# Optimization experiments

Measured on AMD Instinct MI355X. Metric: run time of the kernel, lower is better.

## Reference

```python
import jax, jax.numpy as jnp
import numpy as np

H, HK, D, WIN = 16, 4, 128, 1024  # n_head, n_kv_head, head_dim, left window


def rmsnorm(x):
    eps = jnp.asarray(jnp.finfo(x.dtype).eps, x.dtype)
    return x * jax.lax.rsqrt(jnp.mean(x * x, axis=-1, keepdims=True) + eps)


def rope(x, cos, sin):
    d = x.shape[-1] // 2
    x1, x2 = x[..., :d], x[..., d:]
    return jnp.concatenate([x1 * cos + x2 * sin, x1 * -sin + x2 * cos], axis=-1)


def setup_inputs() -> dict:
    key = jax.random.key(0)
    ks = jax.random.split(key, 12)
    B, T, C = 4, 2048, 2048
    t = jnp.arange(T, dtype=jnp.float32)[:, None]
    inv = 1.0 / (10000.0 ** (jnp.arange(D // 2, dtype=jnp.float32) / (D // 2)))
    ang = t * inv[None, :]  # [T, D/2]
    return {
        "x": jax.random.normal(ks[0], (B, T, C), jnp.float32),
        "x0": jax.random.normal(ks[1], (B, T, C), jnp.float32),
        "ve": jnp.zeros((B, T, C), jnp.float32),  # unused in add_init_qkv branch
        "cos": jnp.cos(ang)[None, :, None, :],  # [1,T,1,D/2]
        "sin": jnp.sin(ang)[None, :, None, :],
        "Wq": jax.random.normal(ks[2], (H * D, C), jnp.float32) * 0.02,
        "Wk": jax.random.normal(ks[3], (HK * D, C), jnp.float32) * 0.02,
        "Wv": jax.random.normal(ks[4], (HK * D, C), jnp.float32) * 0.02,
        "Wproj": jax.random.normal(ks[5], (C, H * D), jnp.float32) * 0.02,
        "alpha_q": jnp.ones((1,), jnp.float32),
        "beta_q": jax.random.uniform(ks[6], (1,), jnp.float32),
        "alpha_k": jnp.ones((1,), jnp.float32),
        "beta_k": jax.random.uniform(ks[7], (1,), jnp.float32),
        "alpha_v": jnp.ones((1,), jnp.float32),
        "beta_v": jax.random.uniform(ks[8], (1,), jnp.float32),
    }


def reference(x, x0, ve, cos, sin, Wq, Wk, Wv, Wproj,
              alpha_q, beta_q, alpha_k, beta_k, alpha_v, beta_v):
    B, T, C = x.shape
    g = H // HK  # GQA group size

    q = (x @ Wq.T).reshape(B, T, H, D)
    k = (x @ Wk.T).reshape(B, T, HK, D)
    v = (x @ Wv.T).reshape(B, T, HK, D)
    v_init = v

    # is_target + add_init_qkv + learn_init_coeffs: blend with projections of norm(x0)
    x0n = rmsnorm(x0)
    cqx = (x0n @ Wq.T).reshape(B, T, H, D)
    ckx = (x0n @ Wk.T).reshape(B, T, HK, D)
    cvx = (x0n @ Wv.T).reshape(B, T, HK, D)
    q = alpha_q * q + beta_q * cqx
    k = alpha_k * k + beta_k * ckx
    v = alpha_v * v + beta_v * cvx

    # rotary + qk-norm + 1.2 scale
    q = rmsnorm(rope(q, cos, sin)) * 1.2
    k = rmsnorm(rope(k, cos, sin)) * 1.2

    qg = q.reshape(B, T, HK, g, D)
    scale = 1.0 / np.sqrt(D)
    scores = jnp.einsum('bqhgd,bkhd->bhgqk', qg, k) * scale  # [B,HK,g,T,T]
    i = jnp.arange(T)[:, None]
    j = jnp.arange(T)[None, :]
    mask = (j <= i) & (i - j <= WIN)
    scores = jnp.where(mask, scores, -jnp.inf)
    p = jax.nn.softmax(scores, axis=-1)
    y = jnp.einsum('bhgqk,bkhd->bqhgd', p, v).reshape(B, T, H * D)

    y = y @ Wproj.T
    return (y, v_init)
```

## Files before the change

### kernel.cpp

```cpp
#include <hip/hip_runtime.h>
#include <hip/hip_bf16.h>
#include <math.h>


using bf16 = __hip_bfloat16;
typedef __attribute__((ext_vector_type(8))) short bf16x8;
typedef __attribute__((ext_vector_type(4))) short bf16x4;
typedef __attribute__((ext_vector_type(4))) float f32x4;

constexpr int Bb = 4, Ts = 2048, Cc = 2048, NH = 16, NKV = 4, Dh = 128, WIN = 1024;
constexpr float EPS = 1.1920929e-07f;

__device__ __forceinline__ void gld16(void* lds, const void* g) {
  __builtin_amdgcn_global_load_lds(
      (__attribute__((address_space(1))) unsigned int*)((void*)g),
      (__attribute__((address_space(3))) unsigned int*)lds, 16, 0, 0);
}

__device__ __forceinline__ unsigned short bfbits(float f) {
  bf16 h = __float2bfloat16(f);
  return __builtin_bit_cast(unsigned short, h);
}

__device__ __forceinline__ void store_out(float* p, float v) { *p = v; }
__device__ __forceinline__ void store_out(bf16* p, float v) { *p = __float2bfloat16(v); }

__device__ __forceinline__ f32x4 mfma16(bf16x4 a, bf16x4 b, f32x4 c) {
#if __has_builtin(__builtin_amdgcn_mfma_f32_16x16x16bf16_1k)
  return __builtin_amdgcn_mfma_f32_16x16x16bf16_1k(a, b, c, 0, 0, 0);
#else
  bf16x8 a8 = {a[0], a[1], a[2], a[3], 0, 0, 0, 0};
  bf16x8 b8 = {b[0], b[1], b[2], b[3], 0, 0, 0, 0};
  return __builtin_amdgcn_mfma_f32_16x16x32_bf16(a8, b8, c, 0, 0, 0);
#endif
}

__global__ __launch_bounds__(256) void convert_w(const float* __restrict__ src,
                                                 bf16* __restrict__ dst, int n4) {
  int i = blockIdx.x * 256 + threadIdx.x;
  if (i < n4) {
    float4 v = ((const float4*)src)[i];
    ushort4 u;
    u.x = bfbits(v.x); u.y = bfbits(v.y); u.z = bfbits(v.z); u.w = bfbits(v.w);
    ((ushort4*)dst)[i] = u;
  }
}

__global__ __launch_bounds__(256) void prep(
    const float* __restrict__ x, const float* __restrict__ x0,
    const float* aq_p, const float* bq_p, const float* ak_p, const float* bk_p,
    bf16* __restrict__ xq, bf16* __restrict__ xk,
    bf16* __restrict__ xb, bf16* __restrict__ x0n) {
  const int row = blockIdx.x, tid = threadIdx.x;
  const float4* xr = (const float4*)(x + (size_t)row * Cc);
  const float4* nr = (const float4*)(x0 + (size_t)row * Cc);
  float4 xa[2], na[2];
  float ss = 0.f;
#pragma unroll
  for (int j = 0; j < 2; ++j) {
    xa[j] = xr[tid + j * 256];
    na[j] = nr[tid + j * 256];
    ss += na[j].x * na[j].x + na[j].y * na[j].y + na[j].z * na[j].z + na[j].w * na[j].w;
  }
#pragma unroll
  for (int o = 32; o; o >>= 1) ss += __shfl_xor(ss, o);
  __shared__ float red[4];
  if ((tid & 63) == 0) red[tid >> 6] = ss;
  __syncthreads();
  const float rms = rsqrtf((red[0] + red[1] + red[2] + red[3]) * (1.f / Cc) + EPS);
  const float aq = *aq_p, bq = *bq_p, ak = *ak_p, bk = *bk_p;
#pragma unroll
  for (int j = 0; j < 2; ++j) {
    const size_t base = (size_t)row * Cc + (size_t)(tid + j * 256) * 4;
    float nx[4] = {na[j].x * rms, na[j].y * rms, na[j].z * rms, na[j].w * rms};
    float xv[4] = {xa[j].x, xa[j].y, xa[j].z, xa[j].w};
    ushort4 uq, uk, ub, un;
    uq.x = bfbits(aq * xv[0] + bq * nx[0]); uq.y = bfbits(aq * xv[1] + bq * nx[1]);
    uq.z = bfbits(aq * xv[2] + bq * nx[2]); uq.w = bfbits(aq * xv[3] + bq * nx[3]);
    uk.x = bfbits(ak * xv[0] + bk * nx[0]); uk.y = bfbits(ak * xv[1] + bk * nx[1]);
    uk.z = bfbits(ak * xv[2] + bk * nx[2]); uk.w = bfbits(ak * xv[3] + bk * nx[3]);
    ub.x = bfbits(xv[0]); ub.y = bfbits(xv[1]); ub.z = bfbits(xv[2]); ub.w = bfbits(xv[3]);
    un.x = bfbits(nx[0]); un.y = bfbits(nx[1]); un.z = bfbits(nx[2]); un.w = bfbits(nx[3]);
    *(ushort4*)(xq + base) = uq;
    *(ushort4*)(xk + base) = uk;
    *(ushort4*)(xb + base) = ub;
    *(ushort4*)(x0n + base) = un;
  }
}

template <typename OutT>
__device__ __forceinline__ void gemm_body(
    const bf16* __restrict__ A, const bf16* __restrict__ W,
    OutT* __restrict__ C, int N, int K) {
  __shared__ unsigned short sA[128 * 64];
  __shared__ unsigned short sB[128 * 64];
  const int tid = threadIdx.x, wave = tid >> 6, lane = tid & 63;
  const int quad = lane >> 4, l15 = lane & 15;
  const int bm = blockIdx.x * 128, bn = blockIdx.y * 128;
  const int wm = (wave >> 1) * 64, wn = (wave & 1) * 64;
  const int srow = wave * 32 + (lane >> 3);
  const int scol = (lane & 7) * 8;

  f32x4 acc[4][4] = {};

  for (int k0 = 0; k0 < K; k0 += 64) {
#pragma unroll
    for (int i = 0; i < 4; ++i) {
      gld16(&sA[(wave * 32 + i * 8) * 64], &A[(size_t)(bm + srow + i * 8) * K + k0 + scol]);
      gld16(&sB[(wave * 32 + i * 8) * 64], &W[(size_t)(bn + srow + i * 8) * K + k0 + scol]);
    }
    __syncthreads();
#pragma unroll
    for (int kk = 0; kk < 2; ++kk) {
      bf16x8 af[4], bfr[4];
#pragma unroll
      for (int t = 0; t < 4; ++t)
        af[t] = *(const bf16x8*)&sA[(wm + t * 16 + l15) * 64 + kk * 32 + quad * 8];
#pragma unroll
      for (int t = 0; t < 4; ++t)
        bfr[t] = *(const bf16x8*)&sB[(wn + t * 16 + l15) * 64 + kk * 32 + quad * 8];
#pragma unroll
      for (int tm = 0; tm < 4; ++tm)
#pragma unroll
        for (int tn = 0; tn < 4; ++tn)
          acc[tm][tn] = __builtin_amdgcn_mfma_f32_16x16x32_bf16(af[tm], bfr[tn], acc[tm][tn], 0, 0, 0);
    }
    __syncthreads();
  }
#pragma unroll
  for (int tm = 0; tm < 4; ++tm)
#pragma unroll
    for (int tn = 0; tn < 4; ++tn)
#pragma unroll
      for (int r = 0; r < 4; ++r) {
        const int row = bm + wm + tm * 16 + quad * 4 + r;
        const int col = bn + wn + tn * 16 + l15;
        store_out(&C[(size_t)row * N + col], acc[tm][tn][r]);
      }
}

template <typename OutT>
__global__ __launch_bounds__(256) void gemm_bt(
    const bf16* __restrict__ A, const bf16* __restrict__ W,
    OutT* __restrict__ C, int N, int K) {
  gemm_body<OutT>(A, W, C, N, K);
}

struct GemmTriple { const bf16* A; const bf16* W; bf16* C; };
struct GemmTriple3 { GemmTriple t[3]; };

__global__ __launch_bounds__(256) void gemm_bt3(GemmTriple3 g, int N, int K) {
  const GemmTriple tr = g.t[blockIdx.z];
  gemm_body<bf16>(tr.A, tr.W, tr.C, N, K);
}

__global__ __launch_bounds__(256) void post_qk(
    const bf16* __restrict__ pre, const float* __restrict__ cosp,
    const float* __restrict__ sinp, bf16* __restrict__ outh, int nh, float mult) {
  const int wid = blockIdx.x * 4 + (threadIdx.x >> 6);
  const int lane = threadIdx.x & 63;
  const int h = wid % nh;
  const int bt = wid / nh;
  const int t = bt & (Ts - 1);
  const int b = bt >> 11;
  const size_t src = (size_t)bt * (size_t)(nh * Dh) + (size_t)h * Dh;
  float x1 = __bfloat162float(pre[src + lane]);
  float x2 = __bfloat162float(pre[src + 64 + lane]);
  float c = cosp[t * 64 + lane], s = sinp[t * 64 + lane];
  float o1 = x1 * c + x2 * s;
  float o2 = x2 * c - x1 * s;
  float ss = o1 * o1 + o2 * o2;
#pragma unroll
  for (int o = 32; o; o >>= 1) ss += __shfl_xor(ss, o);
  const float r = rsqrtf(ss * (1.f / Dh) + EPS) * mult;
  const size_t dst = ((size_t)(b * nh + h) * Ts + t) * Dh;
  outh[dst + lane] = __float2bfloat16(o1 * r);
  outh[dst + 64 + lane] = __float2bfloat16(o2 * r);
}

__global__ __launch_bounds__(256) void post_v(
    const bf16* __restrict__ vinit, const bf16* __restrict__ cvx,
    const float* av_p, const float* bv_p,
    bf16* __restrict__ vth, float* __restrict__ vout) {
  __shared__ unsigned short vt[128 * 65];
  const int t0 = blockIdx.x * 64;
  const int b = blockIdx.y >> 2, hk = blockIdx.y & 3;
  const float av = *av_p, bv = *bv_p;
  const int tid = threadIdx.x;
  for (int j = 0; j < 32; ++j) {
    const int e = j * 256 + tid;
    const int tl = e >> 7, d = e & 127;
    const size_t src = (size_t)(b * Ts + t0 + tl) * (NKV * Dh) + hk * Dh + d;
    const float vi = __bfloat162float(vinit[src]);
    const float cv = __bfloat162float(cvx[src]);
    vout[src] = vi;
    vt[d * 65 + tl] = bfbits(av * vi + bv * cv);
  }
  __syncthreads();
#pragma unroll
  for (int j = 0; j < 4; ++j) {
    const int g = j * 256 + tid;
    const int d = g >> 3, t8 = (g & 7) * 8;
    const unsigned short* p = &vt[d * 65 + t8];
    uint4 u;
    u.x = p[0] | ((unsigned int)p[1] << 16);
    u.y = p[2] | ((unsigned int)p[3] << 16);
    u.z = p[4] | ((unsigned int)p[5] << 16);
    u.w = p[6] | ((unsigned int)p[7] << 16);
    *(uint4*)&vth[((size_t)(b * NKV + hk) * Dh + d) * Ts + t0 + t8] = u;
  }
}

__global__ __launch_bounds__(256) void attn(
    const bf16* __restrict__ qh, const bf16* __restrict__ kh,
    const bf16* __restrict__ vth, bf16* __restrict__ att) {
  __shared__ unsigned short sK[64 * 128];
  __shared__ unsigned short sV[128 * 64];

  const int tid = threadIdx.x, wave = tid >> 6, lane = tid & 63;
  const int quad = lane >> 4, l15 = lane & 15;
  const int q0 = blockIdx.x * 128;
  const int b = blockIdx.y >> 4, h = blockIdx.y & 15, hk = h >> 2;

  const bf16* Qp = qh + (size_t)(b * NH + h) * Ts * Dh;
  const bf16* Kp = kh + (size_t)(b * NKV + hk) * Ts * Dh;
  const bf16* Vp = vth + (size_t)(b * NKV + hk) * Dh * Ts;

  const int qw = q0 + wave * 32;

  bf16x8 qf[2][4];
#pragma unroll
  for (int tm = 0; tm < 2; ++tm)
#pragma unroll
    for (int kk = 0; kk < 4; ++kk)
      qf[tm][kk] = *(const bf16x8*)&Qp[(size_t)(qw + tm * 16 + l15) * Dh + kk * 32 + quad * 8];

  f32x4 of[2][8] = {};
  float m_i[2] = {-__builtin_inff(), -__builtin_inff()};
  float l_i[2] = {0.f, 0.f};

  const int krow = lane >> 4, kgp = lane & 15;
  const int vrow = lane >> 3, vgp = lane & 7;

  const int jt_lo = q0 >= WIN ? (q0 - WIN) >> 6 : 0;
  const int jt_hi = (q0 + 127) >> 6;

  for (int jt = jt_lo; jt <= jt_hi; ++jt) {
    const int j0 = jt << 6;
    __syncthreads();
#pragma unroll
    for (int i = 0; i < 4; ++i) {
      const int row = wave * 16 + i * 4 + krow;
      gld16(&sK[(wave * 16 + i * 4) * 128],
            &Kp[(size_t)(j0 + row) * Dh + (kgp ^ (row & 15)) * 8]);
      const int d = wave * 32 + i * 8 + vrow;
      gld16(&sV[(wave * 32 + i * 8) * 64],
            &Vp[(size_t)d * Ts + j0 + (vgp ^ (d & 7)) * 8]);
    }
    __syncthreads();

    if (j0 > qw + 31 || qw > j0 + 63 + WIN) continue;

    f32x4 sfT[4][2];
#pragma unroll
    for (int tn = 0; tn < 4; ++tn) {
      bf16x8 kf[4];
#pragma unroll
      for (int kk = 0; kk < 4; ++kk)
        kf[kk] = *(const bf16x8*)&sK[(tn * 16 + l15) * 128 + (((kk * 4 + quad) ^ l15) * 8)];
#pragma unroll
      for (int tm = 0; tm < 2; ++tm) {
        f32x4 a = {};
#pragma unroll
        for (int kk = 0; kk < 4; ++kk)
          a = __builtin_amdgcn_mfma_f32_16x16x32_bf16(kf[kk], qf[tm][kk], a, 0, 0, 0);
        sfT[tn][tm] = a;
      }
    }

    float alpha[2];
    bf16x4 pf[2][4];
#pragma unroll
    for (int tm = 0; tm < 2; ++tm) {
      const int dq = (qw + tm * 16 + l15) - (j0 + quad * 4);
      float mloc = -__builtin_inff();
#pragma unroll
      for (int tn = 0; tn < 4; ++tn)
#pragma unroll
        for (int r = 0; r < 4; ++r) {
          const unsigned diff = (unsigned)(dq - tn * 16 - r);
          float s = (diff <= (unsigned)WIN) ? sfT[tn][tm][r] : -__builtin_inff();
          sfT[tn][tm][r] = s;
          mloc = fmaxf(mloc, s);
        }
      mloc = fmaxf(mloc, __shfl_xor(mloc, 16));
      mloc = fmaxf(mloc, __shfl_xor(mloc, 32));
      const float mnew = fmaxf(m_i[tm], mloc);
      alpha[tm] = __builtin_amdgcn_exp2f(m_i[tm] - mnew);
      m_i[tm] = mnew;
      float rs = 0.f;
#pragma unroll
      for (int tn = 0; tn < 4; ++tn) {
        bf16x4 p4;
#pragma unroll
        for (int r = 0; r < 4; ++r) {
          const float p = __builtin_amdgcn_exp2f(sfT[tn][tm][r] - mnew);
          rs += p;
          p4[r] = (short)bfbits(p);
        }
        pf[tm][tn] = p4;
      }
      rs += __shfl_xor(rs, 16);
      rs += __shfl_xor(rs, 32);
      l_i[tm] = l_i[tm] * alpha[tm] + rs;
    }

#pragma unroll
    for (int tm = 0; tm < 2; ++tm) {
      float ar[4];
#pragma unroll
      for (int r = 0; r < 4; ++r) ar[r] = __shfl(alpha[tm], quad * 4 + r);
#pragma unroll
      for (int dn = 0; dn < 8; ++dn)
#pragma unroll
        for (int r = 0; r < 4; ++r) of[tm][dn][r] *= ar[r];
    }

#pragma unroll
    for (int tn = 0; tn < 4; ++tn) {
      const int gsw = (tn * 2) ^ (l15 & 7);
#pragma unroll
      for (int dn = 0; dn < 8; ++dn) {
        const int d = dn * 16 + l15;
        const bf16x4 vf = *(const bf16x4*)&sV[d * 64 + ((gsw ^ (quad >> 1)) * 8) + (quad & 1) * 4];
        of[0][dn] = mfma16(pf[0][tn], vf, of[0][dn]);
        of[1][dn] = mfma16(pf[1][tn], vf, of[1][dn]);
      }
    }
  }

#pragma unroll
  for (int tm = 0; tm < 2; ++tm) {
#pragma unroll
    for (int r = 0; r < 4; ++r) {
      const float lr = __shfl(l_i[tm], quad * 4 + r);
      const float inv = 1.f / lr;
      const int qr = qw + tm * 16 + quad * 4 + r;
      bf16* dst = att + (size_t)(b * Ts + qr) * (NH * Dh) + h * Dh;
#pragma unroll
      for (int dn = 0; dn < 8; ++dn)
        dst[dn * 16 + l15] = __float2bfloat16(of[tm][dn][r] * inv);
    }
  }
}

extern "C" void kernel_launch(void* const* d_in, const int* in_sizes, int n_in,
                              void* d_out, int out_size, void* d_ws, size_t ws_size,
                              hipStream_t stream) {
  const float* x = (const float*)d_in[0];
  const float* x0 = (const float*)d_in[1];
  const float* cosp = (const float*)d_in[3];
  const float* sinp = (const float*)d_in[4];
  const float* Wq = (const float*)d_in[5];
  const float* Wk = (const float*)d_in[6];
  const float* Wv = (const float*)d_in[7];
  const float* Wp = (const float*)d_in[8];
  const float* aq = (const float*)d_in[9];
  const float* bq = (const float*)d_in[10];
  const float* ak = (const float*)d_in[11];
  const float* bk = (const float*)d_in[12];
  const float* av = (const float*)d_in[13];
  const float* bv = (const float*)d_in[14];

  char* ws = (char*)d_ws;
  const size_t MB = 1024ull * 1024;
  bf16* xq = (bf16*)(ws + 0 * MB);
  bf16* xk = (bf16*)(ws + 32 * MB);
  bf16* xb = (bf16*)(ws + 64 * MB);
  bf16* x0n = (bf16*)(ws + 96 * MB);
  bf16* vinit = (bf16*)(ws + 128 * MB);
  bf16* cvx = (bf16*)(ws + 136 * MB);
  bf16* Wqb = (bf16*)(ws + 144 * MB);
  bf16* Wkb = (bf16*)(ws + 152 * MB);
  bf16* Wvb = (bf16*)(ws + 154 * MB);
  bf16* Wpb = (bf16*)(ws + 156 * MB);
  bf16* att = xq;
  bf16* qh = xk;
  bf16* kh = xb;
  bf16* vth = (bf16*)(ws + 72 * MB);

  float* y = (float*)d_out;
  float* vout = (float*)d_out + (size_t)Bb * Ts * Cc;
  bf16* q_pre = (bf16*)d_out;
  bf16* k_pre = (bf16*)vout;

  convert_w<<<4096, 256, 0, stream>>>(Wq, Wqb, 1048576);
  convert_w<<<1024, 256, 0, stream>>>(Wk, Wkb, 262144);
  convert_w<<<1024, 256, 0, stream>>>(Wv, Wvb, 262144);
  convert_w<<<4096, 256, 0, stream>>>(Wp, Wpb, 1048576);

  prep<<<8192, 256, 0, stream>>>(x, x0, aq, bq, ak, bk, xq, xk, xb, x0n);

  gemm_bt<bf16><<<dim3(64, 16), 256, 0, stream>>>(xq, Wqb, q_pre, 2048, 2048);

  GemmTriple3 g3;
  g3.t[0] = {xk, Wkb, k_pre};
  g3.t[1] = {xb, Wvb, vinit};
  g3.t[2] = {x0n, Wvb, cvx};
  gemm_bt3<<<dim3(64, 4, 3), 256, 0, stream>>>(g3, 512, 2048);

  const float qmult = 1.2f * 0.08838834764831845f * 1.4426950408889634f;
  post_qk<<<32768, 256, 0, stream>>>(q_pre, cosp, sinp, qh, NH, qmult);
  post_qk<<<8192, 256, 0, stream>>>(k_pre, cosp, sinp, kh, NKV, 1.2f);
  post_v<<<dim3(32, 16), 256, 0, stream>>>(vinit, cvx, av, bv, vth, vout);

  attn<<<dim3(16, 64), 256, 0, stream>>>(qh, kh, vth, att);

  gemm_bt<float><<<dim3(64, 16), 256, 0, stream>>>(att, Wpb, y, 2048, 2048);
}
```

Baseline: 793.9 us.

## Double-buffer K/V tiles in attention and add lazy softmax rescaling

Makes the attention kernel's K/V shared-memory tiles double-buffered, so the async global-to-LDS load of the next tile overlaps compute on the current one and each iteration needs one barrier instead of two. It also skips masking on tiles that lie entirely inside the window, raises wave priority around the MFMA blocks, and defers the running-max update and output rescale when the new max grows by at most 8 in log2 units. The cost is twice the LDS per block, which may lower occupancy. The deferred rescale lets probabilities reach up to 2^8 before bf16 conversion, a small numerical risk.

```diff
diff --git a/kernel.cpp b/kernel.cpp
--- a/kernel.cpp
+++ b/kernel.cpp
@@ -214,8 +214,8 @@
 __global__ __launch_bounds__(256) void attn(
     const bf16* __restrict__ qh, const bf16* __restrict__ kh,
     const bf16* __restrict__ vth, bf16* __restrict__ att) {
-  __shared__ unsigned short sK[64 * 128];
-  __shared__ unsigned short sV[128 * 64];
+  __shared__ unsigned short sK[2][64 * 128];
+  __shared__ unsigned short sV[2][128 * 64];
 
   const int tid = threadIdx.x, wave = tid >> 6, lane = tid & 63;
   const int quad = lane >> 4, l15 = lane & 15;
@@ -245,98 +245,134 @@
   const int jt_lo = q0 >= WIN ? (q0 - WIN) >> 6 : 0;
   const int jt_hi = (q0 + 127) >> 6;
 
+  auto stage = [&](int jt, int buf) {
+    const int j0s = jt << 6;
+#pragma unroll
+    for (int i = 0; i < 4; ++i) {
+      const int row = wave * 16 + i * 4 + krow;
+      gld16(&sK[buf][(wave * 16 + i * 4) * 128],
+            &Kp[(size_t)(j0s + row) * Dh + (kgp ^ (row & 15)) * 8]);
+      const int d = wave * 32 + i * 8 + vrow;
+      gld16(&sV[buf][(wave * 32 + i * 8) * 64],
+            &Vp[(size_t)d * Ts + j0s + (vgp ^ (d & 7)) * 8]);
+    }
+  };
+
+  int cur = 0;
+  stage(jt_lo, 0);
+  __syncthreads();
+
   for (int jt = jt_lo; jt <= jt_hi; ++jt) {
     const int j0 = jt << 6;
+    if (jt < jt_hi) stage(jt + 1, cur ^ 1);
+
+    if (!(j0 > qw + 31 || qw > j0 + 63 + WIN)) {
+      const unsigned short* kb = sK[cur];
+      const unsigned short* vb = sV[cur];
+
+      f32x4 sfT[4][2];
+      __builtin_amdgcn_s_setprio(1);
+#pragma unroll
+      for (int tn = 0; tn < 4; ++tn) {
+        bf16x8 kf[4];
+#pragma unroll
+        for (int kk = 0; kk < 4; ++kk)
+          kf[kk] = *(const bf16x8*)&kb[(tn * 16 + l15) * 128 + (((kk * 4 + quad) ^ l15) * 8)];
+#pragma unroll
+        for (int tm = 0; tm < 2; ++tm) {
+          f32x4 a = {};
+#pragma unroll
+          for (int kk = 0; kk < 4; ++kk)
+            a = __builtin_amdgcn_mfma_f32_16x16x32_bf16(kf[kk], qf[tm][kk], a, 0, 0, 0);
+          sfT[tn][tm] = a;
+        }
+      }
+      __builtin_amdgcn_s_setprio(0);
+
+      const bool full = (j0 + 63 <= qw) && (qw + 31 - j0 <= WIN);
+
+      float alpha[2];
+      bool defer[2];
+      bf16x4 pf[2][4];
+#pragma unroll
+      for (int tm = 0; tm < 2; ++tm) {
+        float mloc = -__builtin_inff();
+        if (full) {
+#pragma unroll
+          for (int tn = 0; tn < 4; ++tn)
+#pragma unroll
+            for (int r = 0; r < 4; ++r) mloc = fmaxf(mloc, sfT[tn][tm][r]);
+        } else {
+          const int dq = (qw + tm * 16 + l15) - (j0 + quad * 4);
+#pragma unroll
+          for (int tn = 0; tn < 4; ++tn)
+#pragma unroll
+            for (int r = 0; r < 4; ++r) {
+              const unsigned diff = (unsigned)(dq - tn * 16 - r);
+              float s = (diff <= (unsigned)WIN) ? sfT[tn][tm][r] : -__builtin_inff();
+              sfT[tn][tm][r] = s;
+              mloc = fmaxf(mloc, s);
+            }
+        }
+        mloc = fmaxf(mloc, __shfl_xor(mloc, 16));
+        mloc = fmaxf(mloc, __shfl_xor(mloc, 32));
+        defer[tm] = __all(mloc - m_i[tm] <= 8.f);
+        float mnew;
+        if (defer[tm]) {
+          mnew = m_i[tm];
+          alpha[tm] = 1.f;
+        } else {
+          mnew = fmaxf(m_i[tm], mloc);
+          alpha[tm] = __builtin_amdgcn_exp2f(m_i[tm] - mnew);
+          m_i[tm] = mnew;
+        }
+        float rs = 0.f;
+#pragma unroll
+        for (int tn = 0; tn < 4; ++tn) {
+          bf16x4 p4;
+#pragma unroll
+          for (int r = 0; r < 4; ++r) {
+            const float p = __builtin_amdgcn_exp2f(sfT[tn][tm][r] - mnew);
+            rs += p;
+            p4[r] = (short)bfbits(p);
+          }
+          pf[tm][tn] = p4;
+        }
+        rs += __shfl_xor(rs, 16);
+        rs += __shfl_xor(rs, 32);
+        l_i[tm] = l_i[tm] * alpha[tm] + rs;
+      }
+
+#pragma unroll
+      for (int tm = 0; tm < 2; ++tm) {
+        if (!defer[tm]) {
+          float ar[4];
+#pragma unroll
+          for (int r = 0; r < 4; ++r) ar[r] = __shfl(alpha[tm], quad * 4 + r);
+#pragma unroll
+          for (int dn = 0; dn < 8; ++dn)
+#pragma unroll
+            for (int r = 0; r < 4; ++r) of[tm][dn][r] *= ar[r];
+        }
+      }
+
+      __builtin_amdgcn_s_setprio(1);
+#pragma unroll
+      for (int tn = 0; tn < 4; ++tn) {
+        const int gsw = (tn * 2) ^ (l15 & 7);
+#pragma unroll
+        for (int dn = 0; dn < 8; ++dn) {
+          const int d = dn * 16 + l15;
+          const bf16x4 vf = *(const bf16x4*)&vb[d * 64 + ((gsw ^ (quad >> 1)) * 8) + (quad & 1) * 4];
+          of[0][dn] = mfma16(pf[0][tn], vf, of[0][dn]);
+          of[1][dn] = mfma16(pf[1][tn], vf, of[1][dn]);
+        }
+      }
+      __builtin_amdgcn_s_setprio(0);
+    }
+
     __syncthreads();
-#pragma unroll
-    for (int i = 0; i < 4; ++i) {
-      const int row = wave * 16 + i * 4 + krow;
-      gld16(&sK[(wave * 16 + i * 4) * 128],
-            &Kp[(size_t)(j0 + row) * Dh + (kgp ^ (row & 15)) * 8]);
-      const int d = wave * 32 + i * 8 + vrow;
-      gld16(&sV[(wave * 32 + i * 8) * 64],
-            &Vp[(size_t)d * Ts + j0 + (vgp ^ (d & 7)) * 8]);
-    }
-    __syncthreads();
-
-    if (j0 > qw + 31 || qw > j0 + 63 + WIN) continue;
-
-    f32x4 sfT[4][2];
-#pragma unroll
-    for (int tn = 0; tn < 4; ++tn) {
-      bf16x8 kf[4];
-#pragma unroll
-      for (int kk = 0; kk < 4; ++kk)
-        kf[kk] = *(const bf16x8*)&sK[(tn * 16 + l15) * 128 + (((kk * 4 + quad) ^ l15) * 8)];
-#pragma unroll
-      for (int tm = 0; tm < 2; ++tm) {
-        f32x4 a = {};
-#pragma unroll
-        for (int kk = 0; kk < 4; ++kk)
-          a = __builtin_amdgcn_mfma_f32_16x16x32_bf16(kf[kk], qf[tm][kk], a, 0, 0, 0);
-        sfT[tn][tm] = a;
-      }
-    }
-
-    float alpha[2];
-    bf16x4 pf[2][4];
-#pragma unroll
-    for (int tm = 0; tm < 2; ++tm) {
-      const int dq = (qw + tm * 16 + l15) - (j0 + quad * 4);
-      float mloc = -__builtin_inff();
-#pragma unroll
-      for (int tn = 0; tn < 4; ++tn)
-#pragma unroll
-        for (int r = 0; r < 4; ++r) {
-          const unsigned diff = (unsigned)(dq - tn * 16 - r);
-          float s = (diff <= (unsigned)WIN) ? sfT[tn][tm][r] : -__builtin_inff();
-          sfT[tn][tm][r] = s;
-          mloc = fmaxf(mloc, s);
-        }
-      mloc = fmaxf(mloc, __shfl_xor(mloc, 16));
-      mloc = fmaxf(mloc, __shfl_xor(mloc, 32));
-      const float mnew = fmaxf(m_i[tm], mloc);
-      alpha[tm] = __builtin_amdgcn_exp2f(m_i[tm] - mnew);
-      m_i[tm] = mnew;
-      float rs = 0.f;
-#pragma unroll
-      for (int tn = 0; tn < 4; ++tn) {
-        bf16x4 p4;
-#pragma unroll
-        for (int r = 0; r < 4; ++r) {
-          const float p = __builtin_amdgcn_exp2f(sfT[tn][tm][r] - mnew);
-          rs += p;
-          p4[r] = (short)bfbits(p);
-        }
-        pf[tm][tn] = p4;
-      }
-      rs += __shfl_xor(rs, 16);
-      rs += __shfl_xor(rs, 32);
-      l_i[tm] = l_i[tm] * alpha[tm] + rs;
-    }
-
-#pragma unroll
-    for (int tm = 0; tm < 2; ++tm) {
-      float ar[4];
-#pragma unroll
-      for (int r = 0; r < 4; ++r) ar[r] = __shfl(alpha[tm], quad * 4 + r);
-#pragma unroll
-      for (int dn = 0; dn < 8; ++dn)
-#pragma unroll
-        for (int r = 0; r < 4; ++r) of[tm][dn][r] *= ar[r];
-    }
-
-#pragma unroll
-    for (int tn = 0; tn < 4; ++tn) {
-      const int gsw = (tn * 2) ^ (l15 & 7);
-#pragma unroll
-      for (int dn = 0; dn < 8; ++dn) {
-        const int d = dn * 16 + l15;
-        const bf16x4 vf = *(const bf16x4*)&sV[d * 64 + ((gsw ^ (quad >> 1)) * 8) + (quad & 1) * 4];
-        of[0][dn] = mfma16(pf[0][tn], vf, of[0][dn]);
-        of[1][dn] = mfma16(pf[1][tn], vf, of[1][dn]);
-      }
-    }
+    cur ^= 1;
   }
 
 #pragma unroll
```

Measured after the change: 842.7 us. +6.1%, slower.
